# Optimization experiments

Measured on AMD Instinct MI355X. Metric: run time of the kernel, lower is better.

Reference implementation:

```python
import jax, jax.numpy as jnp
import numpy as np
from jax import lax

B, T, I, H, O = 256, 128, 512, 1024, 512


def setup_inputs() -> dict:
    key = jax.random.key(0)
    ks = jax.random.split(key, 7)
    s = 1.0 / np.sqrt(H)  # PyTorch LSTM/Linear init bound
    x = jax.random.normal(ks[0], (B, T, I), dtype=jnp.float32)
    W_ih = jax.random.uniform(ks[1], (4 * H, I), jnp.float32, -s, s)
    W_hh = jax.random.uniform(ks[2], (4 * H, H), jnp.float32, -s, s)
    b_ih = jax.random.uniform(ks[3], (4 * H,), jnp.float32, -s, s)
    b_hh = jax.random.uniform(ks[4], (4 * H,), jnp.float32, -s, s)
    W_fc = jax.random.uniform(ks[5], (O, H), jnp.float32, -s, s)
    b_fc = jax.random.uniform(ks[6], (O,), jnp.float32, -s, s)
    return {"x": x, "W_ih": W_ih, "W_hh": W_hh, "b_ih": b_ih,
            "b_hh": b_hh, "W_fc": W_fc, "b_fc": b_fc}


def _lstm_last(x, W_ih, W_hh, b_ih, b_hh):
    # Precompute input contribution for all timesteps: [T, B, 4H]
    pre = jnp.einsum('bti,gi->tbg', x, W_ih) + b_ih + b_hh

    def step(carry, xg):
        h, c = carry
        gates = xg + h @ W_hh.T  # [B, 4H]
        i, f, g, o = jnp.split(gates, 4, axis=-1)  # PyTorch gate order i,f,g,o
        c = jax.nn.sigmoid(f) * c + jax.nn.sigmoid(i) * jnp.tanh(g)
        h = jax.nn.sigmoid(o) * jnp.tanh(c)
        return (h, c), None

    h0 = jnp.zeros((x.shape[0], W_hh.shape[1]), x.dtype)
    (h, c), _ = lax.scan(step, (h0, h0), pre)
    return h, c


def reference(x, W_ih, W_hh, b_ih, b_hh, W_fc, b_fc):
    h, c = _lstm_last(x, W_ih, W_hh, b_ih, b_hh)
    out = h @ W_fc.T + b_fc  # fc on last timestep hidden
    # hidden returned as (h_n, c_n) with leading n_layers=1 dim, as in PyTorch
    return out, (h[None], c[None])
```

## Files before the change

kernel.cpp:

```cpp
#include <hip/hip_runtime.h>

typedef short bf8 __attribute__((ext_vector_type(8)));
typedef float f32x4 __attribute__((ext_vector_type(4)));
typedef uint u32x4 __attribute__((ext_vector_type(4)));

static constexpr int BB = 256;
static constexpr int TT = 128;
static constexpr int II = 512;
static constexpr int HH = 1024;
static constexpr int OO = 512;
static constexpr int G4 = 4096;
static constexpr int RW = 32;

static constexpr size_t OUT_H = (size_t)BB * OO;
static constexpr size_t OUT_C = OUT_H + (size_t)BB * HH;
static constexpr size_t HBUF  = (size_t)BB * HH;

__device__ __forceinline__ float bf2f(ushort u) {
    unsigned v = ((unsigned)u) << 16;
    return __builtin_bit_cast(float, v);
}
__device__ __forceinline__ ushort f2bf(float f) {
    unsigned x = __builtin_bit_cast(unsigned, f);
    x = x + 0x7FFFu + ((x >> 16) & 1u);
    return (ushort)(x >> 16);
}
__device__ __forceinline__ float sigf(float x) { return 1.0f / (1.0f + __expf(-x)); }
__device__ __forceinline__ float tanhf_(float x) { return 2.0f * sigf(2.0f * x) - 1.0f; }

__device__ __forceinline__ void st_wt_short(const ushort* p, uint v) {
    asm volatile("global_store_short %0, %1, off sc0 sc1" :: "v"(p), "v"(v) : "memory");
}
__device__ __forceinline__ void st_wt_b64(const ushort* p, uint2 v) {
    asm volatile("global_store_dwordx2 %0, %1, off sc0 sc1" :: "v"(p), "v"(v) : "memory");
}
__device__ __forceinline__ void ld_bp_ushort_issue(uint& dst, const ushort* p) {
    asm volatile("global_load_ushort %0, %1, off sc0 sc1" : "=v"(dst) : "v"(p) : "memory");
}
__device__ __forceinline__ void ld_bp_b128_issue(u32x4& dst, const ushort* p) {
    asm volatile("global_load_dwordx4 %0, %1, off sc0 sc1" : "=v"(dst) : "v"(p) : "memory");
}
__device__ __forceinline__ void ld_c_b128_issue(u32x4& dst, const ushort* p) {
    asm volatile("global_load_dwordx4 %0, %1, off" : "=v"(dst) : "v"(p) : "memory");
}
__device__ __forceinline__ void wait_vm0() {
    asm volatile("s_waitcnt vmcnt(0)" ::: "memory");
    __builtin_amdgcn_sched_barrier(0);
}
#define WAITVM(N) do { asm volatile("s_waitcnt vmcnt(" #N ")" ::: "memory"); \
                       __builtin_amdgcn_sched_barrier(0); } while (0)

__device__ __forceinline__ void lightbar(int* slots, int bg, int gen) {
    asm volatile("s_waitcnt vmcnt(0) lgkmcnt(0)" ::: "memory");
    __builtin_amdgcn_sched_barrier(0);
    __syncthreads();
    int tid = threadIdx.x;
    if (tid == 0)
        asm volatile("global_store_dword %0, %1, off sc0 sc1" :: "v"(slots + bg * 32), "v"(gen) : "memory");
    if (tid < 64) {
        const int* sp = slots + tid * 32;
        int v;
        do {
            asm volatile("global_load_dword %0, %1, off sc0 sc1\n\ts_waitcnt vmcnt(0)"
                         : "=v"(v) : "v"(sp) : "memory");
            if (v >= gen) break;
            __builtin_amdgcn_s_sleep(1);
        } while (true);
    }
    __syncthreads();
}

__global__ void k_init(int* flags) {
    int i = blockIdx.x * 256 + threadIdx.x;
    if (i < 8192) flags[i] = 0;
}

__global__ void k_cast(const float* __restrict__ src, ushort* __restrict__ dst, int n4) {
    int i = blockIdx.x * blockDim.x + threadIdx.x;
    int stride = gridDim.x * blockDim.x;
    for (; i < n4; i += stride) {
        float4 v = ((const float4*)src)[i];
        ushort4 o;
        o.x = f2bf(v.x); o.y = f2bf(v.y); o.z = f2bf(v.z); o.w = f2bf(v.w);
        ((ushort4*)dst)[i] = o;
    }
}

__global__ void k_prep_w(const float* __restrict__ w, ushort* __restrict__ wp,
                         const float* __restrict__ bi, const float* __restrict__ bh,
                         float* __restrict__ bp, int Kdim) {
    int p = blockIdx.x;
    int orig = ((p >> 4) & 3) * HH + ((p >> 6) << 4) + (p & 15);
    const float* src = w + (size_t)orig * Kdim;
    ushort* dst = wp + (size_t)p * Kdim;
    for (int k = threadIdx.x; k < Kdim; k += 256) dst[k] = f2bf(src[k]);
    if (threadIdx.x == 0 && bp) bp[p] = bi[orig] + bh[orig];
}

template <int HMODE>
__global__ __launch_bounds__(256) void k_main(
    const float* __restrict__ x, const ushort* __restrict__ wpih,
    const float* __restrict__ bp, ushort* __restrict__ pre,
    const ushort* __restrict__ wphh, ushort* __restrict__ hbf,
    float* __restrict__ dout, int* flags, int SEG) {
    __shared__ ushort wl[32 * 2048];
    __shared__ ushort Al[64 * 32];
    __shared__ ushort Bl[128 * 32];

    int tid = threadIdx.x;
    int bid = blockIdx.x;
    int g = (bid >> 1) & 3;
    int j = ((bid & 1) << 5) | (bid >> 3);
    int row0 = g << 6;
    int* slots = flags + g * 2048;
    int gen = 0;
    int nseg = TT / SEG;

    int w = tid >> 6, l = tid & 63;
    int l15 = l & 15, kg = l >> 4;
    int wbase = ((l15 << 6) + (kg << 4)) ^ ((l15 & 7) << 4);

    {
        const ushort* wsrc = wphh + (size_t)(j << 6) * HH;
        for (int s = 0; s < 32; ++s) {
            int cidx = (s << 8) + tid;
            int c = cidx >> 7;
            int kc = cidx & 127;
            uint4 v = *(const uint4*)(wsrc + (size_t)c * HH + (kc << 3));
            int byte = ((kc >> 2) << 12) + ((((c << 6) + ((kc & 3) << 4))) ^ ((c & 7) << 4));
            *(uint4*)((char*)wl + byte) = v;
        }
        int r = tid >> 2, hc = (tid & 3) << 2;
        uint2 z; z.x = 0; z.y = 0;
        st_wt_b64(hbf + (size_t)(row0 + r) * HH + (j << 4) + hc, z);
    }

    int wm = w >> 1, wn = w & 1;
    int r0 = tid >> 2, kk = tid & 3;
    int sbyteA = ((r0 << 6) + (kk << 4)) ^ ((r0 & 7) << 4);
    int sbyteB1 = sbyteA + 4096;

    const ushort* hbase = hbf + (size_t)(row0 + (w << 4) + l15) * HH + (kg << 3);
    int drow = row0 + (w << 4) + (kg << 2);
    int hcol = (j << 4) + l15;
    ushort* hobase = hbf + (size_t)drow * HH + hcol;
    const ushort* pbase = pre + (size_t)drow * G4 + (j << 6) + l15;
    float creg[4] = {0.f, 0.f, 0.f, 0.f};

    for (int sg = 0; sg < nseg; ++sg) {
        int t0 = sg * SEG;
        int ntiles = SEG << 5;
        for (int q = j; q < ntiles; q += 64) {
            int trel = q >> 5;
            int t = t0 + trel;
            int n0 = (q & 31) << 7;
            const float* xa = x + ((size_t)(row0 + r0) * TT + t) * II + (kk << 3);
            const ushort* gb0 = wpih + (size_t)(n0 + r0) * II + (kk << 3);
            const ushort* gb1 = gb0 + (size_t)64 * II;
            f32x4 acc[2][4];
#pragma unroll
            for (int mi = 0; mi < 2; ++mi)
#pragma unroll
                for (int ni = 0; ni < 4; ++ni) acc[mi][ni] = f32x4{0.f, 0.f, 0.f, 0.f};
            float4 a0 = *(const float4*)xa;
            float4 a1 = *(const float4*)(xa + 4);
            uint4 b0v = *(const uint4*)gb0;
            uint4 b1v = *(const uint4*)gb1;
            for (int ko = 0; ko < 16; ++ko) {
                union { ushort us[8]; uint4 v; } pa;
                pa.us[0] = f2bf(a0.x); pa.us[1] = f2bf(a0.y); pa.us[2] = f2bf(a0.z); pa.us[3] = f2bf(a0.w);
                pa.us[4] = f2bf(a1.x); pa.us[5] = f2bf(a1.y); pa.us[6] = f2bf(a1.z); pa.us[7] = f2bf(a1.w);
                __syncthreads();
                *(uint4*)((char*)Al + sbyteA) = pa.v;
                *(uint4*)((char*)Bl + sbyteA) = b0v;
                *(uint4*)((char*)Bl + sbyteB1) = b1v;
                __syncthreads();
                if (ko < 15) {
                    int k = (ko + 1) << 5;
                    a0 = *(const float4*)(xa + k);
                    a1 = *(const float4*)(xa + k + 4);
                    b0v = *(const uint4*)(gb0 + k);
                    b1v = *(const uint4*)(gb1 + k);
                }
                bf8 af[2], bv[4];
#pragma unroll
                for (int mi = 0; mi < 2; ++mi)
                    af[mi] = *(const bf8*)((char*)Al + wm * 2048 + mi * 1024 + wbase);
#pragma unroll
                for (int ni = 0; ni < 4; ++ni)
                    bv[ni] = *(const bf8*)((char*)Bl + wn * 4096 + ni * 1024 + wbase);
#pragma unroll
                for (int mi = 0; mi < 2; ++mi)
#pragma unroll
                    for (int ni = 0; ni < 4; ++ni)
                        acc[mi][ni] = __builtin_amdgcn_mfma_f32_16x16x32_bf16(af[mi], bv[ni], acc[mi][ni], 0, 0, 0);
            }
#pragma unroll
            for (int ni = 0; ni < 4; ++ni) {
                int col = n0 + wn * 64 + ni * 16 + l15;
                float bias = bp[col];
#pragma unroll
                for (int mi = 0; mi < 2; ++mi) {
                    int arow = row0 + wm * 32 + mi * 16 + (kg << 2);
#pragma unroll
                    for (int r = 0; r < 4; ++r)
                        st_wt_short(pre + ((size_t)trel * BB + arow + r) * G4 + col,
                                    (uint)f2bf(acc[mi][ni][r] + bias));
                }
            }
        }
        gen++; lightbar(slots, j, gen);

        uint prn[16];
#pragma unroll
        for (int ni = 0; ni < 4; ++ni)
#pragma unroll
            for (int r = 0; r < 4; ++r)
                ld_bp_ushort_issue(prn[ni * 4 + r], pbase + (size_t)r * G4 + (ni << 4));
        wait_vm0();

        for (int trel = 0; trel < SEG; ++trel) {
            int t = t0 + trel;
            if (HMODE == 0 && t != 0 && (t & (RW - 1)) == 0)
                __builtin_amdgcn_fence(__ATOMIC_ACQUIRE, "agent");
            int rb = HMODE ? (t & 1) : (t & (RW - 1));
            int wb = HMODE ? ((t & 1) ^ 1) : ((t + 1) & (RW - 1));
            const ushort* hr = hbase + (size_t)rb * HBUF;
            u32x4 xv[8], yv[8];

#define ISSUE8(B, C) \
            _Pragma("unroll") \
            for (int u = 0; u < 8; ++u) { \
                if constexpr (HMODE == 0) ld_c_b128_issue(B[u], hr + (((C) * 8 + u) << 5)); \
                else ld_bp_b128_issue(B[u], hr + (((C) * 8 + u) << 5)); \
            }
#define CONSUME8(B, C) \
            _Pragma("unroll") \
            for (int u = 0; u < 8; ++u) { \
                int ko = (C) * 8 + u; \
                bf8 a = __builtin_bit_cast(bf8, B[u]); \
                _Pragma("unroll") \
                for (int ni = 0; ni < 4; ++ni) { \
                    bf8 b = *(const bf8*)((char*)wl + ko * 4096 + ni * 1024 + wbase); \
                    acc[ni] = __builtin_amdgcn_mfma_f32_16x16x32_bf16(a, b, acc[ni], 0, 0, 0); \
                } \
            }

            f32x4 acc[4];
            ISSUE8(xv, 0)
            ISSUE8(yv, 1)
#pragma unroll
            for (int ni = 0; ni < 4; ++ni)
#pragma unroll
                for (int r = 0; r < 4; ++r) acc[ni][r] = bf2f((ushort)prn[ni * 4 + r]);
            WAITVM(8);
            CONSUME8(xv, 0)
            ISSUE8(xv, 2)
            WAITVM(8);
            CONSUME8(yv, 1)
            ISSUE8(yv, 3)
            WAITVM(8);
            CONSUME8(xv, 2)
            {
                int nrel = (trel + 1 < SEG) ? trel + 1 : 0;
                const ushort* pnn = pre + ((size_t)nrel * BB + drow) * G4 + (j << 6) + l15;
#pragma unroll
                for (int ni = 0; ni < 4; ++ni)
#pragma unroll
                    for (int r = 0; r < 4; ++r)
                        ld_bp_ushort_issue(prn[ni * 4 + r], pnn + (size_t)r * G4 + (ni << 4));
            }
            WAITVM(16);
            CONSUME8(yv, 3)
#undef ISSUE8
#undef CONSUME8

            ushort* ho = hobase + (size_t)wb * HBUF;
            bool last = (t == TT - 1);
#pragma unroll
            for (int r = 0; r < 4; ++r) {
                float ig = sigf(acc[0][r]);
                float fg = sigf(acc[1][r]);
                float gg = tanhf_(acc[2][r]);
                float og = sigf(acc[3][r]);
                float c = fg * creg[r] + ig * gg;
                creg[r] = c;
                float h = og * tanhf_(c);
                st_wt_short(ho + (size_t)r * HH, (uint)f2bf(h));
                if (last) {
                    dout[OUT_H + (size_t)(drow + r) * HH + hcol] = h;
                    dout[OUT_C + (size_t)(drow + r) * HH + hcol] = c;
                }
            }
            gen++; lightbar(slots, j, gen);
        }
    }
}

__global__ __launch_bounds__(256) void k_fc(const ushort* __restrict__ hlast,
                                            const ushort* __restrict__ wfc,
                                            const float* __restrict__ bfc,
                                            float* __restrict__ out) {
    int tid = threadIdx.x;
    int b0 = (blockIdx.x >> 3) << 6;
    int n0 = (blockIdx.x & 7) << 6;
    int w = tid >> 6, l = tid & 63;
    int l15 = l & 15, kg = l >> 4;
    const ushort* ha = hlast + (size_t)(b0 + (w << 4) + l15) * HH + (kg << 3);
    f32x4 acc[4];
#pragma unroll
    for (int ni = 0; ni < 4; ++ni) acc[ni] = f32x4{0.f, 0.f, 0.f, 0.f};
    for (int ko = 0; ko < 32; ++ko) {
        bf8 a = *(const bf8*)(ha + (ko << 5));
#pragma unroll
        for (int ni = 0; ni < 4; ++ni) {
            bf8 b = *(const bf8*)(wfc + (size_t)(n0 + ni * 16 + l15) * HH + (ko << 5) + (kg << 3));
            acc[ni] = __builtin_amdgcn_mfma_f32_16x16x32_bf16(a, b, acc[ni], 0, 0, 0);
        }
    }
    int drow = b0 + (w << 4) + (kg << 2);
#pragma unroll
    for (int ni = 0; ni < 4; ++ni) {
        int col = n0 + ni * 16 + l15;
        float bias = bfc[col];
#pragma unroll
        for (int r = 0; r < 4; ++r)
            out[(size_t)(drow + r) * OO + col] = acc[ni][r] + bias;
    }
}

extern "C" void kernel_launch(void* const* d_in, const int* in_sizes, int n_in,
                              void* d_out, int out_size, void* d_ws, size_t ws_size,
                              hipStream_t stream) {
    const float* x   = (const float*)d_in[0];
    const float* Wih = (const float*)d_in[1];
    const float* Whh = (const float*)d_in[2];
    const float* bih = (const float*)d_in[3];
    const float* bhh = (const float*)d_in[4];
    const float* Wfc = (const float*)d_in[5];
    const float* bfc = (const float*)d_in[6];
    float* out = (float*)d_out;

    char* ws = (char*)d_ws;
    size_t off = 0;
    ushort* wpih = (ushort*)(ws + off); off += (size_t)G4 * II * 2;
    ushort* wphh = (ushort*)(ws + off); off += (size_t)G4 * HH * 2;
    ushort* wfcb = (ushort*)(ws + off); off += (size_t)OO * HH * 2;
    float*  bp   = (float*)(ws + off);  off += (size_t)G4 * 4;
    int*    flags= (int*)(ws + off);    off += 8192 * 4;
    size_t fixed = off;
    size_t HB2 = (size_t)BB * HH * 2;

    int HMODE = 0, SEG = 16;
    size_t hsz = (size_t)RW * HB2;
    while (SEG > 1 && fixed + hsz + (size_t)SEG * BB * G4 * 2 > ws_size) SEG >>= 1;
    if (fixed + hsz + (size_t)SEG * BB * G4 * 2 > ws_size) {
        HMODE = 1; SEG = 16; hsz = 2 * HB2;
        while (SEG > 1 && fixed + hsz + (size_t)SEG * BB * G4 * 2 > ws_size) SEG >>= 1;
    }
    ushort* hbf = (ushort*)(ws + fixed);
    ushort* pre = (ushort*)(ws + fixed + hsz);
    const ushort* hlast = hbf;

    k_init<<<32, 256, 0, stream>>>(flags);
    k_cast<<<256, 256, 0, stream>>>(Wfc, wfcb, OO * HH / 4);
    k_prep_w<<<G4, 256, 0, stream>>>(Wih, wpih, bih, bhh, bp, II);
    k_prep_w<<<G4, 256, 0, stream>>>(Whh, wphh, nullptr, nullptr, nullptr, HH);
    if (HMODE == 0)
        k_main<0><<<256, 256, 0, stream>>>(x, wpih, bp, pre, wphh, hbf, out, flags, SEG);
    else
        k_main<1><<<256, 256, 0, stream>>>(x, wpih, bp, pre, wphh, hbf, out, flags, SEG);
    k_fc<<<32, 256, 0, stream>>>(hlast, wfcb, bfc, out);
}
```

Measured before the change: 1.602 ms.

## Use master-block epoch barrier and coalesce h stores via LDS staging

Replaces the all-to-all flag polling barrier with a two-level scheme. Block 0 of each group waits on all 64 slots and then publishes an epoch word, and the other blocks poll only that single epoch word from one thread. Each step's new h tile is also staged in shared memory and written with 128-bit write-through stores instead of scattered 16-bit stores. The barrier change cuts polling traffic on the slot lines but adds a second hop of latency through the master block. The staging adds a __syncthreads and reuses the Al buffer.

```diff
diff --git a/kernel.cpp b/kernel.cpp
--- a/kernel.cpp
+++ b/kernel.cpp
@@ -34,6 +34,9 @@
 __device__ __forceinline__ void st_wt_b64(const ushort* p, uint2 v) {
     asm volatile("global_store_dwordx2 %0, %1, off sc0 sc1" :: "v"(p), "v"(v) : "memory");
 }
+__device__ __forceinline__ void st_wt_b128(const ushort* p, u32x4 v) {
+    asm volatile("global_store_dwordx4 %0, %1, off sc0 sc1" :: "v"(p), "v"(v) : "memory");
+}
 __device__ __forceinline__ void ld_bp_ushort_issue(uint& dst, const ushort* p) {
     asm volatile("global_load_ushort %0, %1, off sc0 sc1" : "=v"(dst) : "v"(p) : "memory");
 }
@@ -50,21 +53,33 @@
 #define WAITVM(N) do { asm volatile("s_waitcnt vmcnt(" #N ")" ::: "memory"); \
                        __builtin_amdgcn_sched_barrier(0); } while (0)
 
-__device__ __forceinline__ void lightbar(int* slots, int bg, int gen) {
+__device__ __forceinline__ void lightbar2(int* slots, int* epoch, int bg, int gen) {
     asm volatile("s_waitcnt vmcnt(0) lgkmcnt(0)" ::: "memory");
     __builtin_amdgcn_sched_barrier(0);
     __syncthreads();
     int tid = threadIdx.x;
     if (tid == 0)
         asm volatile("global_store_dword %0, %1, off sc0 sc1" :: "v"(slots + bg * 32), "v"(gen) : "memory");
-    if (tid < 64) {
-        const int* sp = slots + tid * 32;
+    if (bg == 0) {
+        if (tid < 64) {
+            const int* sp = slots + tid * 32;
+            int v;
+            do {
+                asm volatile("global_load_dword %0, %1, off sc0 sc1\n\ts_waitcnt vmcnt(0)"
+                             : "=v"(v) : "v"(sp) : "memory");
+                if (v >= gen) break;
+                __builtin_amdgcn_s_sleep(1);
+            } while (true);
+            if (tid == 0)
+                asm volatile("global_store_dword %0, %1, off sc0 sc1" :: "v"(epoch), "v"(gen) : "memory");
+        }
+    } else if (tid == 0) {
         int v;
         do {
             asm volatile("global_load_dword %0, %1, off sc0 sc1\n\ts_waitcnt vmcnt(0)"
-                         : "=v"(v) : "v"(sp) : "memory");
+                         : "=v"(v) : "v"(epoch) : "memory");
             if (v >= gen) break;
-            __builtin_amdgcn_s_sleep(1);
+            __builtin_amdgcn_s_sleep(2);
         } while (true);
     }
     __syncthreads();
@@ -72,7 +87,7 @@
 
 __global__ void k_init(int* flags) {
     int i = blockIdx.x * 256 + threadIdx.x;
-    if (i < 8192) flags[i] = 0;
+    if (i < 8320) flags[i] = 0;
 }
 
 __global__ void k_cast(const float* __restrict__ src, ushort* __restrict__ dst, int n4) {
@@ -113,6 +128,7 @@
     int j = ((bid & 1) << 5) | (bid >> 3);
     int row0 = g << 6;
     int* slots = flags + g * 2048;
+    int* epoch = flags + 8192 + g * 32;
     int gen = 0;
     int nseg = TT / SEG;
 
@@ -143,7 +159,6 @@
     const ushort* hbase = hbf + (size_t)(row0 + (w << 4) + l15) * HH + (kg << 3);
     int drow = row0 + (w << 4) + (kg << 2);
     int hcol = (j << 4) + l15;
-    ushort* hobase = hbf + (size_t)drow * HH + hcol;
     const ushort* pbase = pre + (size_t)drow * G4 + (j << 6) + l15;
     float creg[4] = {0.f, 0.f, 0.f, 0.f};
 
@@ -209,7 +224,7 @@
                 }
             }
         }
-        gen++; lightbar(slots, j, gen);
+        gen++; lightbar2(slots, epoch, j, gen);
 
         uint prn[16];
 #pragma unroll
@@ -275,7 +290,7 @@
 #undef ISSUE8
 #undef CONSUME8
 
-            ushort* ho = hobase + (size_t)wb * HBUF;
+            ushort* hst = Al;
             bool last = (t == TT - 1);
 #pragma unroll
             for (int r = 0; r < 4; ++r) {
@@ -286,13 +301,20 @@
                 float c = fg * creg[r] + ig * gg;
                 creg[r] = c;
                 float h = og * tanhf_(c);
-                st_wt_short(ho + (size_t)r * HH, (uint)f2bf(h));
+                hst[((w << 4) + (kg << 2) + r) * 16 + l15] = f2bf(h);
                 if (last) {
                     dout[OUT_H + (size_t)(drow + r) * HH + hcol] = h;
                     dout[OUT_C + (size_t)(drow + r) * HH + hcol] = c;
                 }
             }
-            gen++; lightbar(slots, j, gen);
+            __syncthreads();
+            if (tid < 128) {
+                u32x4 v = *(const u32x4*)(hst + (tid << 3));
+                const ushort* hop = hbf + (size_t)wb * HBUF
+                                    + (size_t)(row0 + (tid >> 1)) * HH + (j << 4) + ((tid & 1) << 3);
+                st_wt_b128(hop, v);
+            }
+            gen++; lightbar2(slots, epoch, j, gen);
         }
     }
 }
@@ -347,7 +369,7 @@
     ushort* wphh = (ushort*)(ws + off); off += (size_t)G4 * HH * 2;
     ushort* wfcb = (ushort*)(ws + off); off += (size_t)OO * HH * 2;
     float*  bp   = (float*)(ws + off);  off += (size_t)G4 * 4;
-    int*    flags= (int*)(ws + off);    off += 8192 * 4;
+    int*    flags= (int*)(ws + off);    off += 8320 * 4;
     size_t fixed = off;
     size_t HB2 = (size_t)BB * HH * 2;
 
@@ -362,7 +384,7 @@
     ushort* pre = (ushort*)(ws + fixed + hsz);
     const ushort* hlast = hbf;
 
-    k_init<<<32, 256, 0, stream>>>(flags);
+    k_init<<<33, 256, 0, stream>>>(flags);
     k_cast<<<256, 256, 0, stream>>>(Wfc, wfcb, OO * HH / 4);
     k_prep_w<<<G4, 256, 0, stream>>>(Wih, wpih, bih, bhh, bp, II);
     k_prep_w<<<G4, 256, 0, stream>>>(Whh, wphh, nullptr, nullptr, nullptr, HH);
```

New measurement: 1.662 ms. 1.04x slower.

## Replace group barrier with split-phase step flags and double-buffered hidden state

Applied to the files above, without the earlier changes.

Replaces the full store-then-poll lightbar with separate per-step and per-segment flag arrays. Each block publishes its step counter right after writing h and only polls for peers at the start of the next step, so arrival and wait are decoupled. The hidden-state buffer drops from a 32-slot ring to a fixed double buffer read with cache-bypassing loads, which removes the HMODE template and the periodic acquire fences. The cost is more flag traffic, a separate segment barrier, and always paying for bypass loads on h reads.

```diff
diff --git a/kernel.cpp b/kernel.cpp
--- a/kernel.cpp
+++ b/kernel.cpp
@@ -10,7 +10,6 @@
 static constexpr int HH = 1024;
 static constexpr int OO = 512;
 static constexpr int G4 = 4096;
-static constexpr int RW = 32;
 
 static constexpr size_t OUT_H = (size_t)BB * OO;
 static constexpr size_t OUT_C = OUT_H + (size_t)BB * HH;
@@ -40,9 +39,6 @@
 __device__ __forceinline__ void ld_bp_b128_issue(u32x4& dst, const ushort* p) {
     asm volatile("global_load_dwordx4 %0, %1, off sc0 sc1" : "=v"(dst) : "v"(p) : "memory");
 }
-__device__ __forceinline__ void ld_c_b128_issue(u32x4& dst, const ushort* p) {
-    asm volatile("global_load_dwordx4 %0, %1, off" : "=v"(dst) : "v"(p) : "memory");
-}
 __device__ __forceinline__ void wait_vm0() {
     asm volatile("s_waitcnt vmcnt(0)" ::: "memory");
     __builtin_amdgcn_sched_barrier(0);
@@ -50,29 +46,25 @@
 #define WAITVM(N) do { asm volatile("s_waitcnt vmcnt(" #N ")" ::: "memory"); \
                        __builtin_amdgcn_sched_barrier(0); } while (0)
 
-__device__ __forceinline__ void lightbar(int* slots, int bg, int gen) {
-    asm volatile("s_waitcnt vmcnt(0) lgkmcnt(0)" ::: "memory");
+__device__ __forceinline__ void poll_all64(const int* base, int thr) {
+    int l = threadIdx.x & 63;
+    const int* p = base + (l << 5);
+    int v;
+    for (;;) {
+        asm volatile("global_load_dword %0, %1, off sc0 sc1\n\ts_waitcnt vmcnt(0)"
+                     : "=v"(v) : "v"(p) : "memory");
+        if (__all(v >= thr)) break;
+        __builtin_amdgcn_s_sleep(1);
+    }
     __builtin_amdgcn_sched_barrier(0);
-    __syncthreads();
-    int tid = threadIdx.x;
-    if (tid == 0)
-        asm volatile("global_store_dword %0, %1, off sc0 sc1" :: "v"(slots + bg * 32), "v"(gen) : "memory");
-    if (tid < 64) {
-        const int* sp = slots + tid * 32;
-        int v;
-        do {
-            asm volatile("global_load_dword %0, %1, off sc0 sc1\n\ts_waitcnt vmcnt(0)"
-                         : "=v"(v) : "v"(sp) : "memory");
-            if (v >= gen) break;
-            __builtin_amdgcn_s_sleep(1);
-        } while (true);
-    }
-    __syncthreads();
+}
+__device__ __forceinline__ void flag_store(int* slot, int v) {
+    asm volatile("global_store_dword %0, %1, off sc0 sc1" :: "v"(slot), "v"(v) : "memory");
 }
 
 __global__ void k_init(int* flags) {
     int i = blockIdx.x * 256 + threadIdx.x;
-    if (i < 8192) flags[i] = 0;
+    if (i < 16384) flags[i] = 0;
 }
 
 __global__ void k_cast(const float* __restrict__ src, ushort* __restrict__ dst, int n4) {
@@ -97,7 +89,6 @@
     if (threadIdx.x == 0 && bp) bp[p] = bi[orig] + bh[orig];
 }
 
-template <int HMODE>
 __global__ __launch_bounds__(256) void k_main(
     const float* __restrict__ x, const ushort* __restrict__ wpih,
     const float* __restrict__ bp, ushort* __restrict__ pre,
@@ -112,8 +103,10 @@
     int g = (bid >> 1) & 3;
     int j = ((bid & 1) << 5) | (bid >> 3);
     int row0 = g << 6;
-    int* slots = flags + g * 2048;
-    int gen = 0;
+    int* stepf = flags + g * 2048;
+    int* segf  = flags + 8192 + g * 2048;
+    int* mystep = stepf + j * 32;
+    int* myseg  = segf + j * 32;
     int nseg = TT / SEG;
 
     int w = tid >> 6, l = tid & 63;
@@ -134,6 +127,9 @@
         uint2 z; z.x = 0; z.y = 0;
         st_wt_b64(hbf + (size_t)(row0 + r) * HH + (j << 4) + hc, z);
     }
+    wait_vm0();
+    __syncthreads();
+    if (tid == 0) flag_store(mystep, 1);
 
     int wm = w >> 1, wn = w & 1;
     int r0 = tid >> 2, kk = tid & 3;
@@ -149,6 +145,8 @@
 
     for (int sg = 0; sg < nseg; ++sg) {
         int t0 = sg * SEG;
+        if (sg > 0) poll_all64(stepf, t0 + 1);
+
         int ntiles = SEG << 5;
         for (int q = j; q < ntiles; q += 64) {
             int trel = q >> 5;
@@ -209,7 +207,10 @@
                 }
             }
         }
-        gen++; lightbar(slots, j, gen);
+        wait_vm0();
+        __syncthreads();
+        if (tid == 0) flag_store(myseg, sg + 1);
+        poll_all64(segf, sg + 1);
 
         uint prn[16];
 #pragma unroll
@@ -221,19 +222,13 @@
 
         for (int trel = 0; trel < SEG; ++trel) {
             int t = t0 + trel;
-            if (HMODE == 0 && t != 0 && (t & (RW - 1)) == 0)
-                __builtin_amdgcn_fence(__ATOMIC_ACQUIRE, "agent");
-            int rb = HMODE ? (t & 1) : (t & (RW - 1));
-            int wb = HMODE ? ((t & 1) ^ 1) : ((t + 1) & (RW - 1));
-            const ushort* hr = hbase + (size_t)rb * HBUF;
+            poll_all64(stepf, t + 1);
+            const ushort* hr = hbase + (size_t)(t & 1) * HBUF;
             u32x4 xv[8], yv[8];
 
 #define ISSUE8(B, C) \
             _Pragma("unroll") \
-            for (int u = 0; u < 8; ++u) { \
-                if constexpr (HMODE == 0) ld_c_b128_issue(B[u], hr + (((C) * 8 + u) << 5)); \
-                else ld_bp_b128_issue(B[u], hr + (((C) * 8 + u) << 5)); \
-            }
+            for (int u = 0; u < 8; ++u) ld_bp_b128_issue(B[u], hr + (((C) * 8 + u) << 5));
 #define CONSUME8(B, C) \
             _Pragma("unroll") \
             for (int u = 0; u < 8; ++u) { \
@@ -275,7 +270,7 @@
 #undef ISSUE8
 #undef CONSUME8
 
-            ushort* ho = hobase + (size_t)wb * HBUF;
+            ushort* ho = hobase + (size_t)((t & 1) ^ 1) * HBUF;
             bool last = (t == TT - 1);
 #pragma unroll
             for (int r = 0; r < 4; ++r) {
@@ -292,7 +287,9 @@
                     dout[OUT_C + (size_t)(drow + r) * HH + hcol] = c;
                 }
             }
-            gen++; lightbar(slots, j, gen);
+            wait_vm0();
+            __syncthreads();
+            if (tid == 0) flag_store(mystep, t + 2);
         }
     }
 }
@@ -347,28 +344,17 @@
     ushort* wphh = (ushort*)(ws + off); off += (size_t)G4 * HH * 2;
     ushort* wfcb = (ushort*)(ws + off); off += (size_t)OO * HH * 2;
     float*  bp   = (float*)(ws + off);  off += (size_t)G4 * 4;
-    int*    flags= (int*)(ws + off);    off += 8192 * 4;
+    int*    flags= (int*)(ws + off);    off += 16384 * 4;
+    ushort* hbf  = (ushort*)(ws + off); off += (size_t)2 * BB * HH * 2;
     size_t fixed = off;
-    size_t HB2 = (size_t)BB * HH * 2;
-
-    int HMODE = 0, SEG = 16;
-    size_t hsz = (size_t)RW * HB2;
-    while (SEG > 1 && fixed + hsz + (size_t)SEG * BB * G4 * 2 > ws_size) SEG >>= 1;
-    if (fixed + hsz + (size_t)SEG * BB * G4 * 2 > ws_size) {
-        HMODE = 1; SEG = 16; hsz = 2 * HB2;
-        while (SEG > 1 && fixed + hsz + (size_t)SEG * BB * G4 * 2 > ws_size) SEG >>= 1;
-    }
-    ushort* hbf = (ushort*)(ws + fixed);
-    ushort* pre = (ushort*)(ws + fixed + hsz);
-    const ushort* hlast = hbf;
-
-    k_init<<<32, 256, 0, stream>>>(flags);
+    int SEG = 16;
+    while (SEG > 1 && fixed + (size_t)SEG * BB * G4 * 2 > ws_size) SEG >>= 1;
+    ushort* pre = (ushort*)(ws + fixed);
+
+    k_init<<<64, 256, 0, stream>>>(flags);
     k_cast<<<256, 256, 0, stream>>>(Wfc, wfcb, OO * HH / 4);
     k_prep_w<<<G4, 256, 0, stream>>>(Wih, wpih, bih, bhh, bp, II);
     k_prep_w<<<G4, 256, 0, stream>>>(Whh, wphh, nullptr, nullptr, nullptr, HH);
-    if (HMODE == 0)
-        k_main<0><<<256, 256, 0, stream>>>(x, wpih, bp, pre, wphh, hbf, out, flags, SEG);
-    else
-        k_main<1><<<256, 256, 0, stream>>>(x, wpih, bp, pre, wphh, hbf, out, flags, SEG);
-    k_fc<<<32, 256, 0, stream>>>(hlast, wfcb, bfc, out);
-}
+    k_main<<<256, 256, 0, stream>>>(x, wpih, bp, pre, wphh, hbf, out, flags, SEG);
+    k_fc<<<32, 256, 0, stream>>>(hbf, wfcb, bfc, out);
+}
```

New measurement: 1.705 ms. +6.4%, slower.
